# Kernel tuning notes

Hardware: AMD Instinct MI355X
Metric: run time of the kernel (lower is better)

The kernel has to match this reference:

```python
import jax, jax.numpy as jnp
import numpy as np

T, N, E = 4, 20000, 640000
D_IN, D_OUT = 256, 128
RRELU_SLOPE = (1.0 / 8.0 + 1.0 / 3.0) / 2.0  # RReLU eval-mode slope


def setup_inputs() -> dict:
    key = jax.random.key(0)
    ks = jax.random.split(key, 16)

    def glorot(k, shape):
        lim = np.sqrt(6.0 / (shape[0] + shape[1]))
        return jax.random.uniform(k, shape, jnp.float32, -lim, lim)

    node_embs = jax.random.normal(ks[0], (T, N, D_IN), jnp.float32)
    edge_index = jax.random.randint(ks[1], (T, 2, E), 0, N, jnp.int32)
    edge_weight = jax.random.uniform(ks[2], (T, E), jnp.float32)
    mask = jnp.zeros((T, N), jnp.float32)
    return {
        "node_embs": node_embs,
        "edge_index": edge_index,
        "edge_weight": edge_weight,
        "mask": mask,
        "p": glorot(ks[3], (D_IN, 1)),
        "Wz": glorot(ks[4], (D_IN, D_IN)),
        "Uz": glorot(ks[5], (D_IN, D_IN)),
        "bz": jnp.zeros((D_IN, D_OUT), jnp.float32),
        "Wr": glorot(ks[6], (D_IN, D_IN)),
        "Ur": glorot(ks[7], (D_IN, D_IN)),
        "br": jnp.zeros((D_IN, D_OUT), jnp.float32),
        "Wh": glorot(ks[8], (D_IN, D_IN)),
        "Uh": glorot(ks[9], (D_IN, D_IN)),
        "bh": jnp.zeros((D_IN, D_OUT), jnp.float32),
        "W0": glorot(ks[10], (D_IN, D_OUT)),
    }


def reference(node_embs, edge_index, edge_weight, mask, p, Wz, Uz, bz, Wr, Ur, br, Wh, Uh, bh, W0):
    n = node_embs.shape[1]
    k = W0.shape[1]

    def step(W, inputs):
        x, ei, w, m = inputs  # x: [N, D_IN]
        # --- TopK summary (EvolveGCN-H) ---
        scores = (x @ p)[:, 0] / jnp.linalg.norm(p) + m  # [N]
        vals, idx = jax.lax.top_k(scores, k)
        xt = (x[idx] * jnp.tanh(vals)[:, None]).T  # [D_IN, k]
        # --- matrix GRU cell: hidden state is the GCN weight W ---
        z = jax.nn.sigmoid(Wz @ xt + Uz @ W + bz)
        r = jax.nn.sigmoid(Wr @ xt + Ur @ W + br)
        h = jnp.tanh(Wh @ xt + Uh @ (r * W) + bh)
        Wn = (1.0 - z) * W + z * h  # [D_IN, D_OUT]
        # --- sparse GCN conv: adj @ (x @ Wn) ---
        y = x @ Wn  # [N, D_OUT]
        dst, src = ei[0], ei[1]
        agg = jax.ops.segment_sum(w[:, None] * y[src], dst, num_segments=n)
        out = jnp.where(agg >= 0, agg, RRELU_SLOPE * agg)
        return Wn, out

    _, out_seq = jax.lax.scan(step, W0, (node_embs, edge_index, edge_weight, mask))
    return out_seq  # [T, N, D_OUT]
```

## Files before the change

### kernel.cpp

```cpp
#include <hip/hip_runtime.h>

typedef unsigned short u16;
typedef unsigned int u32;
typedef unsigned long long u64;

#define T_ 4
#define N_ 20000
#define E_ 640000
#define DIN 256
#define DOUT 128
#define NT (T_*N_)
#define TE (T_*E_)
#define SLOPE 0.22916666666666666f

#define NB 125
#define BNODES 160
#define CAP 5632
#define NBTOT (T_*NB)

#define SGRAN 11
#define NSB 10
#define NBIN (32*NSB*5)
#define NBIN_PAD 2048
#define BOSTRIDE 40

typedef __attribute__((ext_vector_type(8))) short short8;
typedef __attribute__((ext_vector_type(4))) float f32x4;

__device__ __forceinline__ float blo(u32 u) { return __uint_as_float(u << 16); }
__device__ __forceinline__ float bhi(u32 u) { return __uint_as_float(u & 0xFFFF0000u); }
__device__ __forceinline__ u16 f2bf(float f) {
    u32 u = __float_as_uint(f);
    return (u16)((u + 0x7FFFu + ((u >> 16) & 1u)) >> 16);
}
__device__ __forceinline__ u32 fkey(float f) {
    u32 u = __float_as_uint(f);
    return (u & 0x80000000u) ? ~u : (u | 0x80000000u);
}
__device__ __forceinline__ float fkeyinv(u32 k) {
    u32 u = (k & 0x80000000u) ? (k ^ 0x80000000u) : ~k;
    return __uint_as_float(u);
}

__global__ __launch_bounds__(256) void k_scores(const float* x, const float* p, const float* mask,
                                                float* scores, u16* xb16,
                                                const float* Wz, const float* Uz, const float* Wr,
                                                const float* Ur, const float* Wh, const float* Uh,
                                                u32* Tp) {
    int tid = threadIdx.x;
    if (blockIdx.x >= 5000) {
        int bid = blockIdx.x - 5000;
        int m = bid >> 7, b = bid & 127;
        int idx = b * 256 + tid;
        int d2 = idx & 127, i = idx >> 7;
        const float* src;
        switch (m) {
            case 0: src = Wz; break;
            case 1: src = Uz; break;
            case 2: src = Wr; break;
            case 3: src = Ur; break;
            case 4: src = Wh; break;
            default: src = Uh; break;
        }
        float lo = src[i * 256 + 2 * d2];
        float hi = src[i * 256 + 2 * d2 + 1];
        Tp[m * 32768 + d2 * 256 + i] = (u32)f2bf(lo) | ((u32)f2bf(hi) << 16);
        return;
    }
    __shared__ float pl[256];
    __shared__ float s_invn;
    pl[tid] = p[tid];
    __syncthreads();
    if (tid < 64) {
        float v = pl[tid] * pl[tid] + pl[tid + 64] * pl[tid + 64] +
                  pl[tid + 128] * pl[tid + 128] + pl[tid + 192] * pl[tid + 192];
        for (int o = 32; o > 0; o >>= 1) v += __shfl_xor(v, o);
        if (tid == 0) s_invn = 1.0f / sqrtf(v);
    }
    __syncthreads();
    int wid = tid >> 6, lane = tid & 63;
    for (int it = 0; it < 4; ++it) {
        int node = blockIdx.x * 16 + wid * 4 + it;
        const float* row = x + (size_t)node * DIN + lane * 4;
        float4 u = *(const float4*)row;
        float d = u.x * pl[lane * 4 + 0] + u.y * pl[lane * 4 + 1] +
                  u.z * pl[lane * 4 + 2] + u.w * pl[lane * 4 + 3];
        u32 p0 = (u32)f2bf(u.x) | ((u32)f2bf(u.y) << 16);
        u32 p1 = (u32)f2bf(u.z) | ((u32)f2bf(u.w) << 16);
        *(uint2*)(xb16 + (size_t)node * DIN + lane * 4) = make_uint2(p0, p1);
        for (int o = 32; o > 0; o >>= 1) d += __shfl_xor(d, o);
        if (lane == 0) scores[node] = d * s_invn + mask[node];
    }
}

__global__ __launch_bounds__(256) void k_bin(const int* ei, const float* ew,
                                             int* gcur, uint2* binned) {
    int blk = blockIdx.x;
    int t = blk / 250, ci = blk - t * 250;
    int ebase = ci * 2560;
    int tid = threadIdx.x;
    __shared__ u32 hist[128], sc[128], gbase[128];
    __shared__ uint2 stage[2560];
    if (tid < 128) hist[tid] = 0;
    __syncthreads();
    u32 px[10]; u32 pw[10]; u16 rk[10];
#pragma unroll
    for (int k = 0; k < 10; ++k) {
        int e = ebase + tid + k * 256;
        int dst = ei[t * (2 * E_) + e];
        int src = ei[t * (2 * E_) + E_ + e];
        float w = ew[t * E_ + e];
        int b = dst / BNODES;
        int dl = dst - b * BNODES;
        px[k] = (u32)(t * N_ + src) | ((u32)dl << 17) | ((u32)b << 25);
        pw[k] = __float_as_uint(w);
        rk[k] = (u16)atomicAdd(&hist[b], 1u);
    }
    __syncthreads();
    if (tid < 128) sc[tid] = hist[tid];
    __syncthreads();
    for (int o = 1; o < 128; o <<= 1) {
        u32 v = 0;
        if (tid < 128) { v = sc[tid]; if (tid >= o) v += sc[tid - o]; }
        __syncthreads();
        if (tid < 128) sc[tid] = v;
        __syncthreads();
    }
    if (tid < NB) gbase[tid] = (u32)atomicAdd(&gcur[t * NB + tid], (int)hist[tid]);
#pragma unroll
    for (int k = 0; k < 10; ++k) {
        int b = px[k] >> 25;
        u32 slot = (sc[b] - hist[b]) + rk[k];
        stage[slot] = make_uint2(px[k], pw[k]);
    }
    __syncthreads();
    for (int s = tid; s < 2560; s += 256) {
        uint2 v = stage[s];
        int b = v.x >> 25;
        u32 local = gbase[b] + ((u32)s - (sc[b] - hist[b]));
        if (local < CAP)
            binned[(size_t)(t * NB + b) * CAP + local] = v;
    }
}

__global__ __launch_bounds__(512) void k_scatter(const int* gcur, uint2* binned, int* bandoff) {
    int bg = blockIdx.x;
    int t = bg / NB;
    uint2* bucket = binned + (size_t)bg * CAP;
    int cnt = gcur[bg]; if (cnt > CAP) cnt = CAP;
    int tid = threadIdx.x;
    int tbase = t * N_;
    __shared__ u32 nhist[NBIN_PAD];
    __shared__ u32 binstart[NBIN_PAD];
    __shared__ u32 wsum[8];
    for (int i = tid; i < NBIN_PAD; i += 512) nhist[i] = 0;
    __syncthreads();
    u32 vx[11]; u32 vw[11]; u16 r_[11]; u16 bn_[11];
#pragma unroll
    for (int k = 0; k < 11; ++k) {
        int e = tid + k * 512;
        uint2 v;
        if (e < cnt) {
            v = bucket[e];
        } else {
            v = make_uint2(((u32)(e % BNODES) << 17) | (u32)(tbase + N_ - 1), 0u);
        }
        vx[k] = v.x; vw[k] = v.y;
        int dl = (v.x >> 17) & 255;
        int s = (int)(v.x & 0x1FFFFu) - tbase;
        int bin = (dl / 5) * (NSB * 5) + (s >> SGRAN) * 5 + (dl % 5);
        bn_[k] = (u16)bin;
        r_[k] = (u16)atomicAdd(&nhist[bin], 1u);
    }
    __syncthreads();
    u32 loc1, loc2, loc3, tsum;
    {
        int b0 = tid * 4;
        u32 a = nhist[b0], b = nhist[b0 + 1], c = nhist[b0 + 2], d = nhist[b0 + 3];
        loc1 = a; loc2 = a + b; loc3 = a + b + c; tsum = a + b + c + d;
    }
    int lane = tid & 63, wv = tid >> 6;
    u32 xsc = tsum;
    for (int o = 1; o < 64; o <<= 1) { u32 yv = __shfl_up(xsc, o); if (lane >= o) xsc += yv; }
    if (lane == 63) wsum[wv] = xsc;
    __syncthreads();
    u32 wpre = 0;
    for (int wq = 0; wq < wv; ++wq) wpre += wsum[wq];
    u32 tpre = wpre + xsc - tsum;
    {
        int b0 = tid * 4;
        binstart[b0] = tpre;
        binstart[b0 + 1] = tpre + loc1;
        binstart[b0 + 2] = tpre + loc2;
        binstart[b0 + 3] = tpre + loc3;
    }
    __syncthreads();
    if (tid < 33) {
        int v = (tid < 32) ? (int)binstart[tid * (NSB * 5)] : CAP;
        bandoff[bg * BOSTRIDE + tid] = v;
    }
#pragma unroll
    for (int k = 0; k < 11; ++k) {
        u32 pos = binstart[bn_[k]] + r_[k];
        bucket[pos] = make_uint2(vx[k] & 0x1FFFFFFu, vw[k]);
    }
}

__global__ __launch_bounds__(1024) void k_topk(const float* scores, const float* x, float* xtT) {
    int t = blockIdx.x;
    int tid = threadIdx.x;
    const float* sc = scores + t * N_;
    __shared__ u32 hist[256];
    __shared__ u32 sh_dig, sh_need;
    __shared__ u64 sel[256];
    __shared__ u32 selCount;
    __shared__ u32 idxl[128];
    __shared__ float tvl[128];

    u32 kreg[20];
#pragma unroll
    for (int p = 0; p < 20; ++p) {
        int i = tid + p * 1024;
        kreg[p] = (i < N_) ? fkey(sc[i]) : 0u;
    }

    u32 pref = 0;
    u32 need = 128;
    for (int pass = 0; pass < 4; ++pass) {
        int shift = 24 - 8 * pass;
        if (tid < 256) hist[tid] = 0;
        __syncthreads();
#pragma unroll
        for (int p = 0; p < 20; ++p) {
            int i = tid + p * 1024;
            u32 k = kreg[p];
            bool ok = (i < N_) && ((pass == 0) || ((k >> (shift + 8)) == pref));
            if (ok) atomicAdd(&hist[(k >> shift) & 255u], 1u);
        }
        __syncthreads();
        if (tid < 64) {
            int l = tid;
            u32 s = hist[4 * l] + hist[4 * l + 1] + hist[4 * l + 2] + hist[4 * l + 3];
            u32 S = s;
            for (int o = 1; o < 64; o <<= 1) {
                u32 y = __shfl_down(S, o);
                if (l + o < 64) S += y;
            }
            u64 m = __ballot(S >= need);
            int L = 63 - __builtin_clzll(m);
            if (l == L) {
                u32 Snext = S - s;
                u32 r = 0;
                for (int dd = 3; dd >= 0; --dd) {
                    u32 hb = hist[4 * L + dd];
                    r += hb;
                    if (Snext + r >= need) {
                        sh_dig = (u32)(4 * L + dd);
                        sh_need = need - (Snext + r - hb);
                        break;
                    }
                }
            }
        }
        __syncthreads();
        pref = (pref << 8) | sh_dig;
        need = sh_need;
        __syncthreads();
    }
    if (tid == 0) selCount = 0;
    __syncthreads();
    u32 theta = pref;
#pragma unroll
    for (int p = 0; p < 20; ++p) {
        int i = tid + p * 1024;
        u32 k = kreg[p];
        if (i < N_ && k >= theta) {
            u32 pos = atomicAdd(&selCount, 1u);
            if (pos < 256) sel[pos] = (((u64)(k ^ 0xFFFFFFFFu)) << 32) | (u32)i;
        }
    }
    __syncthreads();
    u32 c = selCount;
    if (c > 256) c = 256;
    if (tid < 256 && (u32)tid >= c) sel[tid] = 0xFFFFFFFFFFFFFFFFull;
    __syncthreads();
    for (int k2 = 2; k2 <= 256; k2 <<= 1) {
        for (int jj = k2 >> 1; jj > 0; jj >>= 1) {
            if (tid < 256) {
                int i = tid, ixj = i ^ jj;
                if (ixj > i) {
                    u64 A = sel[i], B = sel[ixj];
                    bool asc = ((i & k2) == 0);
                    bool sw = asc ? (A > B) : (A < B);
                    if (sw) { sel[i] = B; sel[ixj] = A; }
                }
            }
            __syncthreads();
        }
    }
    if (tid < 128) {
        u64 v = sel[tid];
        u32 k = ((u32)(v >> 32)) ^ 0xFFFFFFFFu;
        idxl[tid] = (u32)(v & 0xFFFFFFFFu);
        tvl[tid] = tanhf(fkeyinv(k));
    }
    __syncthreads();
    float* xt_t = xtT + t * (DIN * DOUT);
    const float* xb = x + (size_t)t * N_ * DIN;
    for (int e2 = tid; e2 < DIN * DOUT; e2 += 1024) {
        int j = e2 >> 8, d = e2 & 255;
        xt_t[e2] = xb[(size_t)idxl[j] * DIN + d] * tvl[j];
    }
}

__global__ __launch_bounds__(1024) void k_gru(const float* xtT, const float* W0, const u32* Tp,
                                              const float* bz, const float* br, const float* bh,
                                              u16* WnT) {
    int j = blockIdx.x;
    int tid = threadIdx.x;
    int i = tid & 255;
    int qk = tid >> 8;
    __shared__ float sxt[256], sW[256], srw[256];
    __shared__ float p1[4][256], p2[4][256];
    const u32* WzT = Tp;
    const u32* UzT = Tp + 32768;
    const u32* WrT = Tp + 65536;
    const u32* UrT = Tp + 98304;
    const u32* WhT = Tp + 131072;
    const u32* UhT = Tp + 163840;
    float wv = W0[i * 128 + j];
    float azb = bz[i * 128 + j];
    float arb = br[i * 128 + j];
    float ahb = bh[i * 128 + j];
    int d2base = qk * 32;
    for (int t = 0; t < T_; ++t) {
        __syncthreads();
        if (qk == 0) {
            sxt[i] = xtT[t * 32768 + j * 256 + i];
            sW[i] = wv;
        }
        __syncthreads();
        float az = 0.f, ar = 0.f;
#pragma unroll 4
        for (int dd = 0; dd < 32; ++dd) {
            int d2 = d2base + dd;
            float x0 = sxt[2 * d2], x1 = sxt[2 * d2 + 1];
            float w0 = sW[2 * d2], w1 = sW[2 * d2 + 1];
            u32 a = WzT[d2 * 256 + i], b = UzT[d2 * 256 + i];
            u32 cc = WrT[d2 * 256 + i], dv = UrT[d2 * 256 + i];
            az += blo(a) * x0 + bhi(a) * x1 + blo(b) * w0 + bhi(b) * w1;
            ar += blo(cc) * x0 + bhi(cc) * x1 + blo(dv) * w0 + bhi(dv) * w1;
        }
        p1[qk][i] = az;
        p2[qk][i] = ar;
        __syncthreads();
        float azs = p1[0][i] + p1[1][i] + p1[2][i] + p1[3][i] + azb;
        float ars = p2[0][i] + p2[1][i] + p2[2][i] + p2[3][i] + arb;
        float z = 1.0f / (1.0f + expf(-azs));
        float r = 1.0f / (1.0f + expf(-ars));
        if (qk == 0) srw[i] = r * wv;
        __syncthreads();
        float ah = 0.f;
#pragma unroll 4
        for (int dd = 0; dd < 32; ++dd) {
            int d2 = d2base + dd;
            float x0 = sxt[2 * d2], x1 = sxt[2 * d2 + 1];
            float r0 = srw[2 * d2], r1 = srw[2 * d2 + 1];
            u32 a = WhT[d2 * 256 + i], b = UhT[d2 * 256 + i];
            ah += blo(a) * x0 + bhi(a) * x1 + blo(b) * r0 + bhi(b) * r1;
        }
        p1[qk][i] = ah;
        __syncthreads();
        float ahs = p1[0][i] + p1[1][i] + p1[2][i] + p1[3][i] + ahb;
        float hh = tanhf(ahs);
        float wn = (1.0f - z) * wv + z * hh;
        if (qk == 0) WnT[t * 32768 + j * 256 + i] = f2bf(wn);
        wv = wn;
    }
}

__global__ __launch_bounds__(128) void k_gemm(const u16* xb16, const u16* WnT, u16* y) {
    int t = blockIdx.y;
    const u16* xb = xb16 + (size_t)t * N_ * DIN;
    const u16* Bt = WnT + t * (DIN * DOUT);
    u16* yb = y + (size_t)t * N_ * DOUT;
    int wid = threadIdx.x >> 6, lane = threadIdx.x & 63;
    int quad = lane >> 4, lm = lane & 15;
    int rowBase = blockIdx.x * 64 + wid * 32;
    f32x4 acc[2][8];
#pragma unroll
    for (int mi = 0; mi < 2; ++mi)
#pragma unroll
        for (int ni = 0; ni < 8; ++ni) acc[mi][ni] = (f32x4){0.f, 0.f, 0.f, 0.f};
    size_t aoff[2];
#pragma unroll
    for (int mi = 0; mi < 2; ++mi) {
        int r = rowBase + mi * 16 + lm;
        if (r > N_ - 1) r = N_ - 1;
        aoff[mi] = (size_t)r * DIN + quad * 8;
    }
    const u16* bbase = Bt + lm * 256 + quad * 8;
    for (int kk = 0; kk < 256; kk += 32) {
        short8 a0 = *(const short8*)(xb + aoff[0] + kk);
        short8 a1 = *(const short8*)(xb + aoff[1] + kk);
#pragma unroll
        for (int ni = 0; ni < 8; ++ni) {
            short8 b = *(const short8*)(bbase + ni * 4096 + kk);
            acc[0][ni] = __builtin_amdgcn_mfma_f32_16x16x32_bf16(a0, b, acc[0][ni], 0, 0, 0);
            acc[1][ni] = __builtin_amdgcn_mfma_f32_16x16x32_bf16(a1, b, acc[1][ni], 0, 0, 0);
        }
    }
#pragma unroll
    for (int mi = 0; mi < 2; ++mi)
#pragma unroll
        for (int ni = 0; ni < 8; ++ni)
#pragma unroll
            for (int r = 0; r < 4; ++r) {
                int row = rowBase + mi * 16 + quad * 4 + r;
                if (row < N_) yb[(size_t)row * DOUT + ni * 16 + lm] = f2bf(acc[mi][ni][r]);
            }
}

__global__ __launch_bounds__(512, 4) void k_agg(const uint2* binned, const int* bandoff,
                                                const u16* y, float* out) {
    int bid = blockIdx.x;
    int xcd = bid & 7;
    int t = xcd >> 1;
    int bl = ((bid >> 3) << 1) + (xcd & 1);
    if (bl >= NB) return;
    int bg = t * NB + bl;
    const uint2* bucket = binned + (size_t)bg * CAP;
    const int* bo = bandoff + bg * BOSTRIDE;
    int w = threadIdx.x >> 6, lane = threadIdx.x & 63;
    int q = lane >> 4, lq = lane & 15;
    int Q = (w << 2) | q;
    __shared__ float acc[BNODES][DOUT];
#pragma unroll
    for (int r = 0; r < 20; ++r)
        *(float2*)&acc[w * 20 + r][2 * lane] = make_float2(0.f, 0.f);
    const u16* yq = y + lq * 8;
    int e = bo[Q];
    int eend = bo[Q + 1];
    int curdl = -1;
    float a0 = 0.f, a1 = 0.f, a2 = 0.f, a3 = 0.f, a4 = 0.f, a5 = 0.f, a6 = 0.f, a7 = 0.f;

#define PROC(mm, vv)                                                    \
    {                                                                   \
        int dl = (int)((mm.x >> 17) & 255u);                            \
        if (dl != curdl) {                                              \
            if (curdl >= 0) {                                           \
                float4* rp = (float4*)&acc[curdl][lq * 8];              \
                float4 r0 = rp[0], r1 = rp[1];                          \
                r0.x += a0; r0.y += a1; r0.z += a2; r0.w += a3;         \
                r1.x += a4; r1.y += a5; r1.z += a6; r1.w += a7;         \
                rp[0] = r0; rp[1] = r1;                                 \
            }                                                           \
            a0 = a1 = a2 = a3 = a4 = a5 = a6 = a7 = 0.f;                \
            curdl = dl;                                                 \
        }                                                               \
        float wt = __uint_as_float(mm.y);                               \
        a0 += wt * blo(vv.x); a1 += wt * bhi(vv.x);                     \
        a2 += wt * blo(vv.y); a3 += wt * bhi(vv.y);                     \
        a4 += wt * blo(vv.z); a5 += wt * bhi(vv.z);                     \
        a6 += wt * blo(vv.w); a7 += wt * bhi(vv.w);                     \
    }

    for (; e + 8 <= eend; e += 8) {
        uint2 m0 = bucket[e];
        uint2 m1 = bucket[e + 1];
        uint2 m2 = bucket[e + 2];
        uint2 m3 = bucket[e + 3];
        uint2 m4 = bucket[e + 4];
        uint2 m5 = bucket[e + 5];
        uint2 m6 = bucket[e + 6];
        uint2 m7 = bucket[e + 7];
        uint4 v0 = *(const uint4*)(yq + (size_t)(m0.x & 0x1FFFFu) * DOUT);
        uint4 v1 = *(const uint4*)(yq + (size_t)(m1.x & 0x1FFFFu) * DOUT);
        uint4 v2 = *(const uint4*)(yq + (size_t)(m2.x & 0x1FFFFu) * DOUT);
        uint4 v3 = *(const uint4*)(yq + (size_t)(m3.x & 0x1FFFFu) * DOUT);
        uint4 v4 = *(const uint4*)(yq + (size_t)(m4.x & 0x1FFFFu) * DOUT);
        uint4 v5 = *(const uint4*)(yq + (size_t)(m5.x & 0x1FFFFu) * DOUT);
        uint4 v6 = *(const uint4*)(yq + (size_t)(m6.x & 0x1FFFFu) * DOUT);
        uint4 v7 = *(const uint4*)(yq + (size_t)(m7.x & 0x1FFFFu) * DOUT);
        PROC(m0, v0)
        PROC(m1, v1)
        PROC(m2, v2)
        PROC(m3, v3)
        PROC(m4, v4)
        PROC(m5, v5)
        PROC(m6, v6)
        PROC(m7, v7)
    }
    for (; e + 4 <= eend; e += 4) {
        uint2 m0 = bucket[e];
        uint2 m1 = bucket[e + 1];
        uint2 m2 = bucket[e + 2];
        uint2 m3 = bucket[e + 3];
        uint4 v0 = *(const uint4*)(yq + (size_t)(m0.x & 0x1FFFFu) * DOUT);
        uint4 v1 = *(const uint4*)(yq + (size_t)(m1.x & 0x1FFFFu) * DOUT);
        uint4 v2 = *(const uint4*)(yq + (size_t)(m2.x & 0x1FFFFu) * DOUT);
        uint4 v3 = *(const uint4*)(yq + (size_t)(m3.x & 0x1FFFFu) * DOUT);
        PROC(m0, v0)
        PROC(m1, v1)
        PROC(m2, v2)
        PROC(m3, v3)
    }
    for (; e < eend; ++e) {
        uint2 m = bucket[e];
        uint4 v = *(const uint4*)(yq + (size_t)(m.x & 0x1FFFFu) * DOUT);
        PROC(m, v)
    }
    if (curdl >= 0) {
        float4* rp = (float4*)&acc[curdl][lq * 8];
        float4 r0 = rp[0], r1 = rp[1];
        r0.x += a0; r0.y += a1; r0.z += a2; r0.w += a3;
        r1.x += a4; r1.y += a5; r1.z += a6; r1.w += a7;
        rp[0] = r0; rp[1] = r1;
    }
#undef PROC
    int gbase = t * N_ + bl * BNODES + w * 20;
#pragma unroll
    for (int r = 0; r < 20; ++r) {
        float v0 = acc[w * 20 + r][2 * lane], v1 = acc[w * 20 + r][2 * lane + 1];
        v0 = (v0 >= 0.f) ? v0 : SLOPE * v0;
        v1 = (v1 >= 0.f) ? v1 : SLOPE * v1;
        *(float2*)(out + (size_t)(gbase + r) * DOUT + 2 * lane) = make_float2(v0, v1);
    }
}

extern "C" void kernel_launch(void* const* d_in, const int* in_sizes, int n_in,
                              void* d_out, int out_size, void* d_ws, size_t ws_size,
                              hipStream_t stream) {
    const float* x = (const float*)d_in[0];
    const int* ei = (const int*)d_in[1];
    const float* ew = (const float*)d_in[2];
    const float* mask = (const float*)d_in[3];
    const float* p = (const float*)d_in[4];
    const float* Wz = (const float*)d_in[5];
    const float* Uz = (const float*)d_in[6];
    const float* bz = (const float*)d_in[7];
    const float* Wr = (const float*)d_in[8];
    const float* Ur = (const float*)d_in[9];
    const float* br = (const float*)d_in[10];
    const float* Wh = (const float*)d_in[11];
    const float* Uh = (const float*)d_in[12];
    const float* bh = (const float*)d_in[13];
    const float* W0 = (const float*)d_in[14];
    float* out = (float*)d_out;

    char* w = (char*)d_ws;
    u16* xb16 = (u16*)w;        w += (size_t)NT * DIN * 2;
    float* scores = (float*)w;  w += 320256;
    float* xtT = (float*)w;     w += 4 * 32768 * 4;
    u16* WnT = (u16*)w;         w += 4 * 32768 * 2;
    u32* Tp = (u32*)w;          w += 6 * 32768 * 4;
    u16* y = (u16*)w;           w += (size_t)NT * DOUT * 2;
    uint2* binned = (uint2*)w;  w += (size_t)NBTOT * CAP * 8;
    int* gcur = (int*)w;        w += 2048;
    int* bandoff = (int*)w;     w += NBTOT * BOSTRIDE * 4;

    hipMemsetAsync(gcur, 0, 2048, stream);

    k_scores<<<5768, 256, 0, stream>>>(x, p, mask, scores, xb16, Wz, Uz, Wr, Ur, Wh, Uh, Tp);
    k_bin<<<1000, 256, 0, stream>>>(ei, ew, gcur, binned);
    k_scatter<<<NBTOT, 512, 0, stream>>>(gcur, binned, bandoff);
    k_topk<<<4, 1024, 0, stream>>>(scores, x, xtT);
    k_gru<<<128, 1024, 0, stream>>>(xtT, W0, Tp, bz, br, bh, WnT);
    k_gemm<<<dim3(313, 4), 128, 0, stream>>>(xb16, WnT, y);
    k_agg<<<512, 512, 0, stream>>>(binned, bandoff, y, out);
}
```

Baseline: 386.5 us.

## Fuse top-k into scatter kernel and sort edges per destination node

The top-k selection kernel is folded into the scatter launch as four extra 512-thread blocks, which removes one kernel launch and lets top-k run alongside the edge scatter. The scatter binning now orders edges by destination node first and source band second, and it emits per-node offsets (BOSTRIDE widened to 168). The aggregation kernel therefore walks exactly five destination nodes per quad with plain register accumulators, which drops the per-edge destination-change check and the read-modify-write into shared memory. In exchange, the top-k blocks hold 40 keys per thread in registers, which may raise register pressure for the whole fused kernel.

```diff
diff --git a/kernel.cpp b/kernel.cpp
--- a/kernel.cpp
+++ b/kernel.cpp
@@ -20,9 +20,9 @@
 
 #define SGRAN 11
 #define NSB 10
-#define NBIN (32*NSB*5)
+#define NBIN (32*5*NSB)
 #define NBIN_PAD 2048
-#define BOSTRIDE 40
+#define BOSTRIDE 168
 
 typedef __attribute__((ext_vector_type(8))) short short8;
 typedef __attribute__((ext_vector_type(4))) float f32x4;
@@ -143,12 +143,117 @@
     }
 }
 
-__global__ __launch_bounds__(512) void k_scatter(const int* gcur, uint2* binned, int* bandoff) {
+__global__ __launch_bounds__(512) void k_scatter(const int* gcur, uint2* binned, int* bandoff,
+                                                 const float* scores, const float* x, float* xtT) {
     int bg = blockIdx.x;
+    int tid = threadIdx.x;
+    if (bg >= NBTOT) {
+        int t = bg - NBTOT;
+        const float* sc = scores + t * N_;
+        __shared__ u32 hist[256];
+        __shared__ u32 sh_dig, sh_need;
+        __shared__ u64 sel[256];
+        __shared__ u32 selCount;
+        __shared__ u32 idxl[128];
+        __shared__ float tvl[128];
+        u32 kreg[40];
+#pragma unroll
+        for (int p = 0; p < 40; ++p) {
+            int i = tid + p * 512;
+            kreg[p] = (i < N_) ? fkey(sc[i]) : 0u;
+        }
+        u32 pref = 0;
+        u32 need = 128;
+        for (int pass = 0; pass < 4; ++pass) {
+            int shift = 24 - 8 * pass;
+            if (tid < 256) hist[tid] = 0;
+            __syncthreads();
+#pragma unroll
+            for (int p = 0; p < 40; ++p) {
+                int i = tid + p * 512;
+                u32 k = kreg[p];
+                bool ok = (i < N_) && ((pass == 0) || ((k >> (shift + 8)) == pref));
+                if (ok) atomicAdd(&hist[(k >> shift) & 255u], 1u);
+            }
+            __syncthreads();
+            if (tid < 64) {
+                int l = tid;
+                u32 s = hist[4 * l] + hist[4 * l + 1] + hist[4 * l + 2] + hist[4 * l + 3];
+                u32 S = s;
+                for (int o = 1; o < 64; o <<= 1) {
+                    u32 y = __shfl_down(S, o);
+                    if (l + o < 64) S += y;
+                }
+                u64 m = __ballot(S >= need);
+                int L = 63 - __builtin_clzll(m);
+                if (l == L) {
+                    u32 Snext = S - s;
+                    u32 r = 0;
+                    for (int dd = 3; dd >= 0; --dd) {
+                        u32 hb = hist[4 * L + dd];
+                        r += hb;
+                        if (Snext + r >= need) {
+                            sh_dig = (u32)(4 * L + dd);
+                            sh_need = need - (Snext + r - hb);
+                            break;
+                        }
+                    }
+                }
+            }
+            __syncthreads();
+            pref = (pref << 8) | sh_dig;
+            need = sh_need;
+            __syncthreads();
+        }
+        if (tid == 0) selCount = 0;
+        __syncthreads();
+        u32 theta = pref;
+#pragma unroll
+        for (int p = 0; p < 40; ++p) {
+            int i = tid + p * 512;
+            u32 k = kreg[p];
+            if (i < N_ && k >= theta) {
+                u32 pos = atomicAdd(&selCount, 1u);
+                if (pos < 256) sel[pos] = (((u64)(k ^ 0xFFFFFFFFu)) << 32) | (u32)i;
+            }
+        }
+        __syncthreads();
+        u32 c = selCount;
+        if (c > 256) c = 256;
+        if (tid < 256 && (u32)tid >= c) sel[tid] = 0xFFFFFFFFFFFFFFFFull;
+        __syncthreads();
+        for (int k2 = 2; k2 <= 256; k2 <<= 1) {
+            for (int jj = k2 >> 1; jj > 0; jj >>= 1) {
+                if (tid < 256) {
+                    int i = tid, ixj = i ^ jj;
+                    if (ixj > i) {
+                        u64 A = sel[i], B = sel[ixj];
+                        bool asc = ((i & k2) == 0);
+                        bool sw = asc ? (A > B) : (A < B);
+                        if (sw) { sel[i] = B; sel[ixj] = A; }
+                    }
+                }
+                __syncthreads();
+            }
+        }
+        if (tid < 128) {
+            u64 v = sel[tid];
+            u32 k = ((u32)(v >> 32)) ^ 0xFFFFFFFFu;
+            idxl[tid] = (u32)(v & 0xFFFFFFFFu);
+            tvl[tid] = tanhf(fkeyinv(k));
+        }
+        __syncthreads();
+        float* xt_t = xtT + t * (DIN * DOUT);
+        const float* xb = x + (size_t)t * N_ * DIN;
+        for (int e2 = tid; e2 < DIN * DOUT; e2 += 512) {
+            int j = e2 >> 8, d = e2 & 255;
+            xt_t[e2] = xb[(size_t)idxl[j] * DIN + d] * tvl[j];
+        }
+        return;
+    }
     int t = bg / NB;
     uint2* bucket = binned + (size_t)bg * CAP;
     int cnt = gcur[bg]; if (cnt > CAP) cnt = CAP;
-    int tid = threadIdx.x;
     int tbase = t * N_;
     __shared__ u32 nhist[NBIN_PAD];
     __shared__ u32 binstart[NBIN_PAD];
@@ -168,7 +273,7 @@
         vx[k] = v.x; vw[k] = v.y;
         int dl = (v.x >> 17) & 255;
         int s = (int)(v.x & 0x1FFFFu) - tbase;
-        int bin = (dl / 5) * (NSB * 5) + (s >> SGRAN) * 5 + (dl % 5);
+        int bin = (dl / 5) * (5 * NSB) + (dl % 5) * NSB + (s >> SGRAN);
         bn_[k] = (u16)bin;
         r_[k] = (u16)atomicAdd(&nhist[bin], 1u);
     }
@@ -195,121 +300,14 @@
         binstart[b0 + 3] = tpre + loc3;
     }
     __syncthreads();
-    if (tid < 33) {
-        int v = (tid < 32) ? (int)binstart[tid * (NSB * 5)] : CAP;
+    if (tid < 161) {
+        int v = (tid < 160) ? (int)binstart[tid * NSB] : CAP;
         bandoff[bg * BOSTRIDE + tid] = v;
     }
 #pragma unroll
     for (int k = 0; k < 11; ++k) {
         u32 pos = binstart[bn_[k]] + r_[k];
         bucket[pos] = make_uint2(vx[k] & 0x1FFFFFFu, vw[k]);
-    }
-}
-
-__global__ __launch_bounds__(1024) void k_topk(const float* scores, const float* x, float* xtT) {
-    int t = blockIdx.x;
-    int tid = threadIdx.x;
-    const float* sc = scores + t * N_;
-    __shared__ u32 hist[256];
-    __shared__ u32 sh_dig, sh_need;
-    __shared__ u64 sel[256];
-    __shared__ u32 selCount;
-    __shared__ u32 idxl[128];
-    __shared__ float tvl[128];
-
-    u32 kreg[20];
-#pragma unroll
-    for (int p = 0; p < 20; ++p) {
-        int i = tid + p * 1024;
-        kreg[p] = (i < N_) ? fkey(sc[i]) : 0u;
-    }
-
-    u32 pref = 0;
-    u32 need = 128;
-    for (int pass = 0; pass < 4; ++pass) {
-        int shift = 24 - 8 * pass;
-        if (tid < 256) hist[tid] = 0;
-        __syncthreads();
-#pragma unroll
-        for (int p = 0; p < 20; ++p) {
-            int i = tid + p * 1024;
-            u32 k = kreg[p];
-            bool ok = (i < N_) && ((pass == 0) || ((k >> (shift + 8)) == pref));
-            if (ok) atomicAdd(&hist[(k >> shift) & 255u], 1u);
-        }
-        __syncthreads();
-        if (tid < 64) {
-            int l = tid;
-            u32 s = hist[4 * l] + hist[4 * l + 1] + hist[4 * l + 2] + hist[4 * l + 3];
-            u32 S = s;
-            for (int o = 1; o < 64; o <<= 1) {
-                u32 y = __shfl_down(S, o);
-                if (l + o < 64) S += y;
-            }
-            u64 m = __ballot(S >= need);
-            int L = 63 - __builtin_clzll(m);
-            if (l == L) {
-                u32 Snext = S - s;
-                u32 r = 0;
-                for (int dd = 3; dd >= 0; --dd) {
-                    u32 hb = hist[4 * L + dd];
-                    r += hb;
-                    if (Snext + r >= need) {
-                        sh_dig = (u32)(4 * L + dd);
-                        sh_need = need - (Snext + r - hb);
-                        break;
-                    }
-                }
-            }
-        }
-        __syncthreads();
-        pref = (pref << 8) | sh_dig;
-        need = sh_need;
-        __syncthreads();
-    }
-    if (tid == 0) selCount = 0;
-    __syncthreads();
-    u32 theta = pref;
-#pragma unroll
-    for (int p = 0; p < 20; ++p) {
-        int i = tid + p * 1024;
-        u32 k = kreg[p];
-        if (i < N_ && k >= theta) {
-            u32 pos = atomicAdd(&selCount, 1u);
-            if (pos < 256) sel[pos] = (((u64)(k ^ 0xFFFFFFFFu)) << 32) | (u32)i;
-        }
-    }
-    __syncthreads();
-    u32 c = selCount;
-    if (c > 256) c = 256;
-    if (tid < 256 && (u32)tid >= c) sel[tid] = 0xFFFFFFFFFFFFFFFFull;
-    __syncthreads();
-    for (int k2 = 2; k2 <= 256; k2 <<= 1) {
-        for (int jj = k2 >> 1; jj > 0; jj >>= 1) {
-            if (tid < 256) {
-                int i = tid, ixj = i ^ jj;
-                if (ixj > i) {
-                    u64 A = sel[i], B = sel[ixj];
-                    bool asc = ((i & k2) == 0);
-                    bool sw = asc ? (A > B) : (A < B);
-                    if (sw) { sel[i] = B; sel[ixj] = A; }
-                }
-            }
-            __syncthreads();
-        }
-    }
-    if (tid < 128) {
-        u64 v = sel[tid];
-        u32 k = ((u32)(v >> 32)) ^ 0xFFFFFFFFu;
-        idxl[tid] = (u32)(v & 0xFFFFFFFFu);
-        tvl[tid] = tanhf(fkeyinv(k));
-    }
-    __syncthreads();
-    float* xt_t = xtT + t * (DIN * DOUT);
-    const float* xb = x + (size_t)t * N_ * DIN;
-    for (int e2 = tid; e2 < DIN * DOUT; e2 += 1024) {
-        int j = e2 >> 8, d = e2 & 255;
-        xt_t[e2] = xb[(size_t)idxl[j] * DIN + d] * tvl[j];
     }
 }
 
@@ -435,29 +433,10 @@
     int q = lane >> 4, lq = lane & 15;
     int Q = (w << 2) | q;
     __shared__ float acc[BNODES][DOUT];
-#pragma unroll
-    for (int r = 0; r < 20; ++r)
-        *(float2*)&acc[w * 20 + r][2 * lane] = make_float2(0.f, 0.f);
     const u16* yq = y + lq * 8;
-    int e = bo[Q];
-    int eend = bo[Q + 1];
-    int curdl = -1;
-    float a0 = 0.f, a1 = 0.f, a2 = 0.f, a3 = 0.f, a4 = 0.f, a5 = 0.f, a6 = 0.f, a7 = 0.f;
-
-#define PROC(mm, vv)                                                    \
+
+#define FMA8(mm, vv)                                                    \
     {                                                                   \
-        int dl = (int)((mm.x >> 17) & 255u);                            \
-        if (dl != curdl) {                                              \
-            if (curdl >= 0) {                                           \
-                float4* rp = (float4*)&acc[curdl][lq * 8];              \
-                float4 r0 = rp[0], r1 = rp[1];                          \
-                r0.x += a0; r0.y += a1; r0.z += a2; r0.w += a3;         \
-                r1.x += a4; r1.y += a5; r1.z += a6; r1.w += a7;         \
-                rp[0] = r0; rp[1] = r1;                                 \
-            }                                                           \
-            a0 = a1 = a2 = a3 = a4 = a5 = a6 = a7 = 0.f;                \
-            curdl = dl;                                                 \
-        }                                                               \
         float wt = __uint_as_float(mm.y);                               \
         a0 += wt * blo(vv.x); a1 += wt * bhi(vv.x);                     \
         a2 += wt * blo(vv.y); a3 += wt * bhi(vv.y);                     \
@@ -465,59 +444,48 @@
         a6 += wt * blo(vv.w); a7 += wt * bhi(vv.w);                     \
     }
 
-    for (; e + 8 <= eend; e += 8) {
-        uint2 m0 = bucket[e];
-        uint2 m1 = bucket[e + 1];
-        uint2 m2 = bucket[e + 2];
-        uint2 m3 = bucket[e + 3];
-        uint2 m4 = bucket[e + 4];
-        uint2 m5 = bucket[e + 5];
-        uint2 m6 = bucket[e + 6];
-        uint2 m7 = bucket[e + 7];
-        uint4 v0 = *(const uint4*)(yq + (size_t)(m0.x & 0x1FFFFu) * DOUT);
-        uint4 v1 = *(const uint4*)(yq + (size_t)(m1.x & 0x1FFFFu) * DOUT);
-        uint4 v2 = *(const uint4*)(yq + (size_t)(m2.x & 0x1FFFFu) * DOUT);
-        uint4 v3 = *(const uint4*)(yq + (size_t)(m3.x & 0x1FFFFu) * DOUT);
-        uint4 v4 = *(const uint4*)(yq + (size_t)(m4.x & 0x1FFFFu) * DOUT);
-        uint4 v5 = *(const uint4*)(yq + (size_t)(m5.x & 0x1FFFFu) * DOUT);
-        uint4 v6 = *(const uint4*)(yq + (size_t)(m6.x & 0x1FFFFu) * DOUT);
-        uint4 v7 = *(const uint4*)(yq + (size_t)(m7.x & 0x1FFFFu) * DOUT);
-        PROC(m0, v0)
-        PROC(m1, v1)
-        PROC(m2, v2)
-        PROC(m3, v3)
-        PROC(m4, v4)
-        PROC(m5, v5)
-        PROC(m6, v6)
-        PROC(m7, v7)
-    }
-    for (; e + 4 <= eend; e += 4) {
-        uint2 m0 = bucket[e];
-        uint2 m1 = bucket[e + 1];
-        uint2 m2 = bucket[e + 2];
-        uint2 m3 = bucket[e + 3];
-        uint4 v0 = *(const uint4*)(yq + (size_t)(m0.x & 0x1FFFFu) * DOUT);
-        uint4 v1 = *(const uint4*)(yq + (size_t)(m1.x & 0x1FFFFu) * DOUT);
-        uint4 v2 = *(const uint4*)(yq + (size_t)(m2.x & 0x1FFFFu) * DOUT);
-        uint4 v3 = *(const uint4*)(yq + (size_t)(m3.x & 0x1FFFFu) * DOUT);
-        PROC(m0, v0)
-        PROC(m1, v1)
-        PROC(m2, v2)
-        PROC(m3, v3)
-    }
-    for (; e < eend; ++e) {
-        uint2 m = bucket[e];
-        uint4 v = *(const uint4*)(yq + (size_t)(m.x & 0x1FFFFu) * DOUT);
-        PROC(m, v)
-    }
-    if (curdl >= 0) {
-        float4* rp = (float4*)&acc[curdl][lq * 8];
-        float4 r0 = rp[0], r1 = rp[1];
-        r0.x += a0; r0.y += a1; r0.z += a2; r0.w += a3;
-        r1.x += a4; r1.y += a5; r1.z += a6; r1.w += a7;
-        rp[0] = r0; rp[1] = r1;
-    }
-#undef PROC
+#pragma unroll
+    for (int d = 0; d < 5; ++d) {
+        int e = bo[Q * 5 + d];
+        int eend = bo[Q * 5 + d + 1];
+        float a0 = 0.f, a1 = 0.f, a2 = 0.f, a3 = 0.f;
+        float a4 = 0.f, a5 = 0.f, a6 = 0.f, a7 = 0.f;
+        for (; e + 8 <= eend; e += 8) {
+            uint2 m0 = bucket[e];
+            uint2 m1 = bucket[e + 1];
+            uint2 m2 = bucket[e + 2];
+            uint2 m3 = bucket[e + 3];
+            uint2 m4 = bucket[e + 4];
+            uint2 m5 = bucket[e + 5];
+            uint2 m6 = bucket[e + 6];
+            uint2 m7 = bucket[e + 7];
+            uint4 v0 = *(const uint4*)(yq + (size_t)(m0.x & 0x1FFFFu) * DOUT);
+            uint4 v1 = *(const uint4*)(yq + (size_t)(m1.x & 0x1FFFFu) * DOUT);
+            uint4 v2 = *(const uint4*)(yq + (size_t)(m2.x & 0x1FFFFu) * DOUT);
+            uint4 v3 = *(const uint4*)(yq + (size_t)(m3.x & 0x1FFFFu) * DOUT);
+            uint4 v4 = *(const uint4*)(yq + (size_t)(m4.x & 0x1FFFFu) * DOUT);
+            uint4 v5 = *(const uint4*)(yq + (size_t)(m5.x & 0x1FFFFu) * DOUT);
+            uint4 v6 = *(const uint4*)(yq + (size_t)(m6.x & 0x1FFFFu) * DOUT);
+            uint4 v7 = *(const uint4*)(yq + (size_t)(m7.x & 0x1FFFFu) * DOUT);
+            FMA8(m0, v0)
+            FMA8(m1, v1)
+            FMA8(m2, v2)
+            FMA8(m3, v3)
+            FMA8(m4, v4)
+            FMA8(m5, v5)
+            FMA8(m6, v6)
+            FMA8(m7, v7)
+        }
+        for (; e < eend; ++e) {
+            uint2 m = bucket[e];
+            uint4 v = *(const uint4*)(yq + (size_t)(m.x & 0x1FFFFu) * DOUT);
+            FMA8(m, v)
+        }
+        float4* rp = (float4*)&acc[Q * 5 + d][lq * 8];
+        rp[0] = make_float4(a0, a1, a2, a3);
+        rp[1] = make_float4(a4, a5, a6, a7);
+    }
+#undef FMA8
     int gbase = t * N_ + bl * BNODES + w * 20;
 #pragma unroll
     for (int r = 0; r < 20; ++r) {
@@ -563,8 +531,7 @@
 
     k_scores<<<5768, 256, 0, stream>>>(x, p, mask, scores, xb16, Wz, Uz, Wr, Ur, Wh, Uh, Tp);
     k_bin<<<1000, 256, 0, stream>>>(ei, ew, gcur, binned);
-    k_scatter<<<NBTOT, 512, 0, stream>>>(gcur, binned, bandoff);
-    k_topk<<<4, 1024, 0, stream>>>(scores, x, xtT);
+    k_scatter<<<NBTOT + 4, 512, 0, stream>>>(gcur, binned, bandoff, scores, x, xtT);
     k_gru<<<128, 1024, 0, stream>>>(xtT, W0, Tp, bz, br, bh, WnT);
     k_gemm<<<dim3(313, 4), 128, 0, stream>>>(xb16, WnT, y);
     k_agg<<<512, 512, 0, stream>>>(binned, bandoff, y, out);
```

After: 380.6 us. About the same (-1.5%).
